# Performance work log

Hardware: AMD Instinct MI355X
Metric: run time of the kernel (lower is better)

The kernel has to match this reference:

```python
import jax, jax.numpy as jnp
import numpy as np

B, CIN, H, W = 4, 64, 128, 128
COUT, K, S, P = 64, 3, 1, 1


def setup_inputs() -> dict:
    key = jax.random.key(0)
    k1, k2, k3, k4 = jax.random.split(key, 4)
    x = jax.random.normal(k1, (B, CIN, H, W), jnp.float32)
    # offset-predicting conv params (small scale so offsets stay in a sane range)
    offset_w = jax.random.normal(k2, (2 * K * K, CIN, K, K), jnp.float32) * 0.01
    offset_b = jnp.zeros((2 * K * K,), jnp.float32)
    # deformable conv params
    fan_in = CIN * K * K
    deform_w = jax.random.normal(k3, (COUT, CIN, K, K), jnp.float32) / np.sqrt(fan_in).astype(np.float32)
    deform_b = jax.random.normal(k4, (COUT,), jnp.float32) * 0.01
    return {"x": x, "offset_w": offset_w, "offset_b": offset_b,
            "deform_w": deform_w, "deform_b": deform_b}


def _conv2d(x, w, b, stride, pad):
    y = jax.lax.conv_general_dilated(
        x, w, window_strides=(stride, stride),
        padding=[(pad, pad), (pad, pad)],
        dimension_numbers=("NCHW", "OIHW", "NCHW"))
    return y + b[None, :, None, None]


def _deform_conv2d(x, offset, w, b, stride, pad):
    Bn, C, Hi, Wi = x.shape
    O, _, Kh, Kw = w.shape
    KK = Kh * Kw
    Ho = (Hi + 2 * pad - Kh) // stride + 1
    Wo = (Wi + 2 * pad - Kw) // stride + 1
    # offset layout (torchvision/mmcv): [B, KK, 2, Ho, Wo] with (dy, dx)
    off = offset.reshape(Bn, KK, 2, Ho, Wo)
    dy, dx = off[:, :, 0], off[:, :, 1]
    ky, kx = jnp.meshgrid(jnp.arange(Kh), jnp.arange(Kw), indexing="ij")
    ky = ky.reshape(-1).astype(x.dtype)  # [KK]
    kx = kx.reshape(-1).astype(x.dtype)
    hgrid = (jnp.arange(Ho) * stride - pad).astype(x.dtype)  # [Ho]
    wgrid = (jnp.arange(Wo) * stride - pad).astype(x.dtype)  # [Wo]
    # fractional sampling coords [B, KK, Ho, Wo]
    ys = hgrid[None, None, :, None] + ky[None, :, None, None] + dy
    xs = wgrid[None, None, None, :] + kx[None, :, None, None] + dx
    y0 = jnp.floor(ys)
    x0 = jnp.floor(xs)
    ly = (ys - y0)[:, None]  # [B,1,KK,Ho,Wo] for channel broadcast
    lx = (xs - x0)[:, None]
    y0i = y0.astype(jnp.int32)
    x0i = x0.astype(jnp.int32)

    def samp(yi, xi):
        valid = (yi >= 0) & (yi < Hi) & (xi >= 0) & (xi < Wi)
        yc = jnp.clip(yi, 0, Hi - 1)
        xc = jnp.clip(xi, 0, Wi - 1)
        # per-batch gather -> [B, C, KK, Ho, Wo]
        v = jax.vmap(lambda im, yy, xx: im[:, yy, xx])(x, yc, xc)
        return v * valid[:, None].astype(x.dtype)

    v00 = samp(y0i, x0i)
    v01 = samp(y0i, x0i + 1)
    v10 = samp(y0i + 1, x0i)
    v11 = samp(y0i + 1, x0i + 1)
    sampled = (v00 * (1 - ly) * (1 - lx) + v01 * (1 - ly) * lx
               + v10 * ly * (1 - lx) + v11 * ly * lx)  # [B,C,KK,Ho,Wo]
    out = jnp.einsum("bckhw,ock->bohw", sampled, w.reshape(O, C, KK))
    return out + b[None, :, None, None]


def reference(x, offset_w, offset_b, deform_w, deform_b):
    offset = _conv2d(x, offset_w, offset_b, S, P)
    return _deform_conv2d(x, offset, deform_w, deform_b, S, P)
```

## Files before the change

### kernel.cpp

```cpp
#include <hip/hip_runtime.h>
#include <hip/hip_bf16.h>

#define B_    4
#define CIN_  64
#define H_    128
#define W_    128
#define COUT_ 64
#define KK_   9
#define OFFC_ 18
#define HW_   (H_*W_)
#define TILE_ 64

typedef _Float16 hf8 __attribute__((ext_vector_type(8)));
typedef float f32x4  __attribute__((ext_vector_type(4)));

__device__ inline _Float16 f2h(float f) { return (_Float16)f; }

__global__ __launch_bounds__(256) void prep_all(
    const float* __restrict__ x,
    const float* __restrict__ ow, const float* __restrict__ dw,
    _Float16* __restrict__ xt, _Float16* __restrict__ dwh, _Float16* __restrict__ owh)
{
    __shared__ _Float16 t[64 * 66];
    const int tid = threadIdx.x;
    const int bid = blockIdx.x;
    if (bid < 1024) {
        const int b    = bid >> 8;
        const int pb   = bid & 255;
        const int pix0 = pb * 64;
        const int p    = tid & 63;
        const int g    = tid >> 6;
        const float* src = x + ((size_t)b * CIN_ + g * 16) * HW_ + pix0 + p;
        #pragma unroll
        for (int j = 0; j < 16; ++j)
            t[p * 66 + g * 16 + j] = f2h(src[(size_t)j * HW_]);
        __syncthreads();
        #pragma unroll
        for (int k = 0; k < 2; ++k) {
            const int p2  = k * 32 + (tid >> 3);
            const int sub = tid & 7;
            _Float16 vals[8];
            #pragma unroll
            for (int j = 0; j < 8; ++j) vals[j] = t[p2 * 66 + sub * 8 + j];
            *(hf8*)&xt[((size_t)b * HW_ + pix0 + p2) * 64 + sub * 8] = *(hf8*)vals;
        }
    } else {
        const int idx = (bid - 1024) * 256 + tid;
        {
            const int k = idx / (COUT_ * CIN_);
            const int r = idx % (COUT_ * CIN_);
            const int o = r >> 6, c = r & 63;
            dwh[idx] = f2h(dw[(o * CIN_ + c) * KK_ + k]);
        }
        if (idx < KK_ * 32 * CIN_) {
            const int k = idx / (32 * CIN_);
            const int r = idx % (32 * CIN_);
            const int co = r >> 6, c = r & 63;
            owh[idx] = f2h(co < OFFC_ ? ow[(co * CIN_ + c) * KK_ + k] : 0.0f);
        }
    }
}

#define DECL_SET(S) \
    hf8 r00a##S, r00b##S, r01a##S, r01b##S, r10a##S, r10b##S, r11a##S, r11b##S; \
    float pm0##S, pm1##S, pm2##S, pm3##S;

#define LOAD_SET(S, t) { \
    const int ky = (t) / 3, kx = (t) % 3; \
    const float dy = offs[(2 * (t) + 0) * TILE_ + p]; \
    const float dx = offs[(2 * (t) + 1) * TILE_ + p]; \
    const float ys = (float)(ho + ky - 1) + dy; \
    const float xs = (float)(wo + kx - 1) + dx; \
    const float y0f = floorf(ys), x0f = floorf(xs); \
    const float ly = ys - y0f, lx = xs - x0f; \
    const int y0 = (int)y0f, x0 = (int)x0f; \
    const int y1 = y0 + 1,   x1 = x0 + 1; \
    const bool y0v = (y0 >= 0) & (y0 < H_); \
    const bool y1v = (y1 >= 0) & (y1 < H_); \
    const bool x0v = (x0 >= 0) & (x0 < W_); \
    const bool x1v = (x1 >= 0) & (x1 < W_); \
    pm0##S = (y0v & x0v) ? (1.f - ly) * (1.f - lx) : 0.f; \
    pm1##S = (y0v & x1v) ? (1.f - ly) * lx         : 0.f; \
    pm2##S = (y1v & x0v) ? ly * (1.f - lx)         : 0.f; \
    pm3##S = (y1v & x1v) ? ly * lx                 : 0.f; \
    const int y0c = min(max(y0, 0), H_ - 1); \
    const int y1c = min(max(y1, 0), H_ - 1); \
    const int x0c = min(max(x0, 0), W_ - 1); \
    const int x1c = min(max(x1, 0), W_ - 1); \
    const _Float16* c00 = xbt + (size_t)(y0c * W_ + x0c) * 64 + sub * 8; \
    const _Float16* c01 = xbt + (size_t)(y0c * W_ + x1c) * 64 + sub * 8; \
    const _Float16* c10 = xbt + (size_t)(y1c * W_ + x0c) * 64 + sub * 8; \
    const _Float16* c11 = xbt + (size_t)(y1c * W_ + x1c) * 64 + sub * 8; \
    r00a##S = *(const hf8*)(c00); r00b##S = *(const hf8*)(c00 + 32); \
    r01a##S = *(const hf8*)(c01); r01b##S = *(const hf8*)(c01 + 32); \
    r10a##S = *(const hf8*)(c10); r10b##S = *(const hf8*)(c10 + 32); \
    r11a##S = *(const hf8*)(c11); r11b##S = *(const hf8*)(c11 + 32); \
}

#define COMBINE_WRITE(S, dstbuf) { \
    const hf8 m00v = (hf8)f2h(pm0##S); \
    const hf8 m01v = (hf8)f2h(pm1##S); \
    const hf8 m10v = (hf8)f2h(pm2##S); \
    const hf8 m11v = (hf8)f2h(pm3##S); \
    const hf8 va = m00v * r00a##S + m01v * r01a##S + m10v * r10a##S + m11v * r11a##S; \
    const hf8 vb = m00v * r00b##S + m01v * r01b##S + m10v * r10b##S + m11v * r11b##S; \
    const int cA = sub; \
    const int cB = sub + 4; \
    *(hf8*)&u.smp[(dstbuf) * 4096 + p * 64 + ((cA ^ (p & 7)) << 3)] = va; \
    *(hf8*)&u.smp[(dstbuf) * 4096 + p * 64 + ((cB ^ (p & 7)) << 3)] = vb; \
}

__global__ __launch_bounds__(256, 4) void fused_deform_mfma(
    const _Float16* __restrict__ xt,
    const _Float16* __restrict__ owh,
    const float* __restrict__ obias,
    const _Float16* __restrict__ dwh,
    const float* __restrict__ dbias,
    float* __restrict__ out)
{
    __shared__ union {
        _Float16 xtl[3 * 66 * 64];
        _Float16 smp[4 * 64 * 64];
    } u;
    __shared__ float offs[OFFC_ * TILE_];

    const int lin  = blockIdx.x;
    const int nid  = (lin & 7) * 128 + (lin >> 3);
    const int b    = nid >> 8;
    const int tile = nid & 255;

    const int tid = threadIdx.x;
    const int pixbase = tile * TILE_;
    const int ho    = pixbase >> 7;
    const int wbase = pixbase & (W_ - 1);
    const int lane  = tid & 63;
    const int wv    = tid >> 6;
    const int arow  = lane & 15;
    const int kseg  = lane >> 4;

    const _Float16* xbt = xt + (size_t)b * HW_ * 64;

    for (int base = 0; base < 3 * 66 * 8; base += 256) {
        const int idx = base + tid;
        if (idx < 3 * 66 * 8) {
            const int cc = idx & 7;
            const int qy = idx >> 3;
            const int y  = qy / 66;
            const int q  = qy - y * 66;
            const int gy = ho + y - 1;
            const int gx = wbase + q - 1;
            hf8 v;
            if (gy >= 0 && gy < H_ && gx >= 0 && gx < W_) {
                v = *(const hf8*)&xbt[(size_t)(gy * W_ + gx) * 64 + cc * 8];
            } else {
                v = (hf8)(_Float16)0.0f;
            }
            *(hf8*)&u.xtl[(y * 66 + q) * 64 + ((cc ^ (q & 7)) << 3)] = v;
        }
    }
    __syncthreads();

    {
        const int m = wv & 1;
        const int h = wv >> 1;
        f32x4 acca[2];
        acca[0] = (f32x4)0.f; acca[1] = (f32x4)0.f;
        for (int t = 0; t < KK_; ++t) {
            const int ky = t / 3, kx = t % 3;
            #pragma unroll
            for (int kc = 0; kc < 2; ++kc) {
                const int cbase = kc * 32 + kseg * 8;
                const hf8 afrag = *(const hf8*)&owh[(t * 32 + m * 16 + arow) * 64 + cbase];
                const int cchunk = cbase >> 3;
                #pragma unroll
                for (int nt = 0; nt < 2; ++nt) {
                    const int pp = h * 32 + nt * 16 + arow;
                    const int q = pp + kx;
                    const hf8 bfrag = *(const hf8*)&u.xtl[(ky * 66 + q) * 64 + ((cchunk ^ (q & 7)) << 3)];
                    acca[nt] = __builtin_amdgcn_mfma_f32_16x16x32_f16(afrag, bfrag, acca[nt], 0, 0, 0);
                }
            }
        }
        #pragma unroll
        for (int nt = 0; nt < 2; ++nt) {
            #pragma unroll
            for (int r = 0; r < 4; ++r) {
                const int co = m * 16 + kseg * 4 + r;
                if (co < OFFC_) {
                    const int pp = h * 32 + nt * 16 + arow;
                    offs[co * TILE_ + pp] = acca[nt][r] + obias[co];
                }
            }
        }
    }
    __syncthreads();

    const int pix16 = lane >> 2;
    const int sub   = lane & 3;
    const int p     = wv * 16 + pix16;
    const int wo    = wbase + p;

    DECL_SET(A)
    DECL_SET(B)

    f32x4 accb[4];
    #pragma unroll
    for (int nt = 0; nt < 4; ++nt) accb[nt] = (f32x4)0.f;

    auto mfmaTap = [&](int t, int srcbuf) {
        #pragma unroll
        for (int kc = 0; kc < 2; ++kc) {
            const int cbase = kc * 32 + kseg * 8;
            const hf8 afrag = *(const hf8*)&dwh[(t * 64 + wv * 16 + arow) * 64 + cbase];
            const int cchunk = cbase >> 3;
            #pragma unroll
            for (int nt = 0; nt < 4; ++nt) {
                const int pp = nt * 16 + arow;
                const hf8 bfrag = *(const hf8*)&u.smp[srcbuf * 4096 + pp * 64 + ((cchunk ^ (pp & 7)) << 3)];
                accb[nt] = __builtin_amdgcn_mfma_f32_16x16x32_f16(afrag, bfrag, accb[nt], 0, 0, 0);
            }
        }
    };

    LOAD_SET(A, 0)
    LOAD_SET(B, 1)
    COMBINE_WRITE(A, 0)
    COMBINE_WRITE(B, 1)
    __syncthreads();

    #pragma unroll
    for (int r = 0; r < 4; ++r) {
        const int ta = 2 * r + 2;
        const int tb = 2 * r + 3;
        const int sb = ((r + 1) & 1) * 2;
        const int cb = (r & 1) * 2;
        LOAD_SET(A, ta)
        if (tb < KK_) LOAD_SET(B, tb)
        mfmaTap(2 * r,     cb + 0);
        mfmaTap(2 * r + 1, cb + 1);
        COMBINE_WRITE(A, sb + 0)
        if (tb < KK_) COMBINE_WRITE(B, sb + 1)
        __syncthreads();
    }
    mfmaTap(8, 0);

    float* ob = out + (size_t)b * COUT_ * HW_ + pixbase;
    #pragma unroll
    for (int nt = 0; nt < 4; ++nt) {
        const int pp = nt * 16 + arow;
        #pragma unroll
        for (int r = 0; r < 4; ++r) {
            const int o = wv * 16 + kseg * 4 + r;
            ob[(size_t)o * HW_ + pp] = accb[nt][r] + dbias[o];
        }
    }
}

extern "C" void kernel_launch(void* const* d_in, const int* in_sizes, int n_in,
                              void* d_out, int out_size, void* d_ws, size_t ws_size,
                              hipStream_t stream) {
    const float* x        = (const float*)d_in[0];
    const float* offset_w = (const float*)d_in[1];
    const float* offset_b = (const float*)d_in[2];
    const float* deform_w = (const float*)d_in[3];
    const float* deform_b = (const float*)d_in[4];
    float* out = (float*)d_out;

    _Float16* dwh = (_Float16*)d_ws;
    _Float16* owh = (_Float16*)((char*)d_ws + 73728);
    _Float16* xt  = (_Float16*)((char*)d_ws + 110592);

    prep_all<<<1024 + 144, 256, 0, stream>>>(x, offset_w, deform_w, xt, dwh, owh);

    fused_deform_mfma<<<1024, 256, 0, stream>>>(xt, owh, offset_b, dwh, deform_b, out);
}
```

Baseline: 44.12 us.

## Keep offset conv results in registers and fetch them via wave shuffles

The offset convolution is remapped so each wave computes all 32 offset channels for its own 16 pixels, with the B fragment reused across both M tiles. The results stay in accumulator registers, and each thread pulls its dy/dx values with __shfl instead of going through a shared-memory offs array. This removes the offs buffer, its stores, one barrier and the LDS reads. The tap loop is spelled out through a switch so the shuffle indices become compile-time constants. A barrier is added before the first sample write because the smp buffer aliases xtl in the union.

```diff
diff --git a/kernel.cpp b/kernel.cpp
--- a/kernel.cpp
+++ b/kernel.cpp
@@ -67,8 +67,9 @@
 
 #define LOAD_SET(S, t) { \
     const int ky = (t) / 3, kx = (t) % 3; \
-    const float dy = offs[(2 * (t) + 0) * TILE_ + p]; \
-    const float dx = offs[(2 * (t) + 1) * TILE_ + p]; \
+    constexpr int coY = 2 * (t), coX = 2 * (t) + 1; \
+    const float dy = __shfl(acca[coY >> 4][coY & 3], ((coY >> 2) & 3) * 16 + pix16); \
+    const float dx = __shfl(acca[coX >> 4][coX & 3], ((coX >> 2) & 3) * 16 + pix16); \
     const float ys = (float)(ho + ky - 1) + dy; \
     const float xs = (float)(wo + kx - 1) + dx; \
     const float y0f = floorf(ys), x0f = floorf(xs); \
@@ -122,7 +123,6 @@
         _Float16 xtl[3 * 66 * 64];
         _Float16 smp[4 * 64 * 64];
     } u;
-    __shared__ float offs[OFFC_ * TILE_];
 
     const int lin  = blockIdx.x;
     const int nid  = (lin & 7) * 128 + (lin >> 3);
@@ -160,40 +160,33 @@
     }
     __syncthreads();
 
+    f32x4 acca[2];
+    acca[0] = (f32x4)0.f; acca[1] = (f32x4)0.f;
     {
-        const int m = wv & 1;
-        const int h = wv >> 1;
-        f32x4 acca[2];
-        acca[0] = (f32x4)0.f; acca[1] = (f32x4)0.f;
+        const int px = wv * 16 + arow;
         for (int t = 0; t < KK_; ++t) {
             const int ky = t / 3, kx = t % 3;
+            const int q  = px + kx;
             #pragma unroll
             for (int kc = 0; kc < 2; ++kc) {
                 const int cbase = kc * 32 + kseg * 8;
-                const hf8 afrag = *(const hf8*)&owh[(t * 32 + m * 16 + arow) * 64 + cbase];
                 const int cchunk = cbase >> 3;
+                const hf8 bfrag = *(const hf8*)&u.xtl[(ky * 66 + q) * 64 + ((cchunk ^ (q & 7)) << 3)];
                 #pragma unroll
-                for (int nt = 0; nt < 2; ++nt) {
-                    const int pp = h * 32 + nt * 16 + arow;
-                    const int q = pp + kx;
-                    const hf8 bfrag = *(const hf8*)&u.xtl[(ky * 66 + q) * 64 + ((cchunk ^ (q & 7)) << 3)];
-                    acca[nt] = __builtin_amdgcn_mfma_f32_16x16x32_f16(afrag, bfrag, acca[nt], 0, 0, 0);
+                for (int m = 0; m < 2; ++m) {
+                    const hf8 afrag = *(const hf8*)&owh[(t * 32 + m * 16 + arow) * 64 + cbase];
+                    acca[m] = __builtin_amdgcn_mfma_f32_16x16x32_f16(afrag, bfrag, acca[m], 0, 0, 0);
                 }
             }
         }
         #pragma unroll
-        for (int nt = 0; nt < 2; ++nt) {
+        for (int m = 0; m < 2; ++m)
             #pragma unroll
             for (int r = 0; r < 4; ++r) {
                 const int co = m * 16 + kseg * 4 + r;
-                if (co < OFFC_) {
-                    const int pp = h * 32 + nt * 16 + arow;
-                    offs[co * TILE_ + pp] = acca[nt][r] + obias[co];
-                }
-            }
-        }
-    }
-    __syncthreads();
+                if (co < OFFC_) acca[m][r] += obias[co];
+            }
+    }
 
     const int pix16 = lane >> 2;
     const int sub   = lane & 3;
@@ -224,18 +217,22 @@
 
     LOAD_SET(A, 0)
     LOAD_SET(B, 1)
+    __syncthreads();
     COMBINE_WRITE(A, 0)
     COMBINE_WRITE(B, 1)
     __syncthreads();
 
     #pragma unroll
     for (int r = 0; r < 4; ++r) {
-        const int ta = 2 * r + 2;
         const int tb = 2 * r + 3;
         const int sb = ((r + 1) & 1) * 2;
         const int cb = (r & 1) * 2;
-        LOAD_SET(A, ta)
-        if (tb < KK_) LOAD_SET(B, tb)
+        switch (r) {
+        case 0: LOAD_SET(A, 2) LOAD_SET(B, 3) break;
+        case 1: LOAD_SET(A, 4) LOAD_SET(B, 5) break;
+        case 2: LOAD_SET(A, 6) LOAD_SET(B, 7) break;
+        case 3: LOAD_SET(A, 8) break;
+        }
         mfmaTap(2 * r,     cb + 0);
         mfmaTap(2 * r + 1, cb + 1);
         COMBINE_WRITE(A, sb + 0)
```

After: 51.82 us. 17.5% more time.
